# Performance work log

Measured on AMD Instinct MI355X. Metric: run time of the kernel, lower is better.

Reference implementation:

```python
import jax, jax.numpy as jnp
import numpy as np

ALPHA = 2.0
K_HOPS = 3
N_NODES, N_EDGES, IN_DIM = 8192, 131072, 128


def _mlp(coeffs, W0, W1, W2, W3):
    # MLP(n_layers=n_hidden_layers+2=4, relu between, no bias, bn/dropout off in eval)
    h = jax.nn.relu(coeffs @ W0)
    h = jax.nn.relu(h @ W1)
    h = jax.nn.relu(h @ W2)
    return h @ W3  # [N, 1] rotation angles


def _aggregate_k_hop(edge_index, angles):
    # Faithful translation of aggregate_k_hop including its in-place aliasing:
    # enhanced_angles aliases angles, and step_k ACCUMULATES across hops
    # (torch_scatter reduces into the provided out tensor).
    N = angles.shape[0]
    row, col = edge_index[0], edge_index[1]
    f = lambda k: jnp.exp(jnp.asarray(-ALPHA * k, angles.dtype))
    # hop 1: scatter-add over the raw edge list (duplicate edges counted, as in original)
    step = jax.ops.segment_sum(angles[col] * f(1), row, num_segments=N)
    enhanced = angles + step
    # Dense boolean adjacency: composing paths then np.unique(axis=1) is exactly the
    # 'exists a k-step walk' indicator, i.e. boolean adjacency powers.
    adj = jnp.zeros((N, N), jnp.float32).at[row, col].set(1.0)
    P = adj
    for k in range(2, K_HOPS + 1):
        P = ((P @ adj) > 0).astype(jnp.float32)  # unique k-walk pairs
        step = step + f(k) * (P @ enhanced)      # reads angles AFTER previous in-place add
        enhanced = enhanced + step               # step accumulates across hops
    return enhanced


def setup_inputs() -> dict:
    key = jax.random.key(0)
    k0, k1, k2, k3, k4, k5 = jax.random.split(key, 6)
    s = 1.0 / np.sqrt(IN_DIM)
    return {
        "coeffs": jax.random.normal(k0, (N_NODES, IN_DIM), jnp.float32),
        "W0": jax.random.normal(k1, (IN_DIM, IN_DIM), jnp.float32) * s,
        "W1": jax.random.normal(k2, (IN_DIM, IN_DIM), jnp.float32) * s,
        "W2": jax.random.normal(k3, (IN_DIM, IN_DIM), jnp.float32) * s,
        "W3": jax.random.normal(k4, (IN_DIM, 1), jnp.float32) * s,
        "edge_index": jax.random.randint(k5, (2, N_EDGES), 0, N_NODES, dtype=jnp.int32),
    }


def reference(coeffs, W0, W1, W2, W3, edge_index):
    angles = _mlp(coeffs, W0, W1, W2, W3)
    return _aggregate_k_hop(edge_index, angles)  # batch.node_rotation_angles, [N, 1]
```

## Files before the change

kernel.cpp:

```cpp
#include <hip/hip_runtime.h>

constexpr int N    = 8192;
constexpr int NE   = 131072;
constexpr int WPR  = N / 32;
constexpr int MAXD = 64;

#define F1 0.13533528323661270f
#define F2 0.018315638888734179f
#define F3 0.0024787521766663585f

using bf16x8 = __attribute__((ext_vector_type(8))) short;
using f32x4  = __attribute__((ext_vector_type(4))) float;

__device__ __forceinline__ unsigned short f2bf(float f) {
    unsigned int u = __float_as_uint(f);
    u = (u + 0x7FFFu + ((u >> 16) & 1u)) >> 16;
    return (unsigned short)u;
}

__global__ __launch_bounds__(256) void mlp_kernel(
    const float* __restrict__ X,
    const float* __restrict__ W0, const float* __restrict__ W1,
    const float* __restrict__ W2, const float* __restrict__ W3,
    float* __restrict__ angles, float* __restrict__ e1,
    uint4* __restrict__ cntz)
{
    __shared__ unsigned short Xb[32 * 136];
    __shared__ unsigned short Wt[128 * 136];
    __shared__ float part[2][32];

    const int tid  = threadIdx.x;
    const int row0 = blockIdx.x * 32;
    const int w  = tid >> 6, l = tid & 63;
    const int mt = w & 1, nh = w >> 1;
    const int lm = l & 15, lq = l >> 4;

    if (tid < 8) {
        uint4 z; z.x = z.y = z.z = z.w = 0u;
        cntz[blockIdx.x * 8 + tid] = z;
    }

    for (int q = tid; q < 32 * 32; q += 256) {
        float4 v = *(const float4*)&X[row0 * 128 + q * 4];
        ushort4 b;
        b.x = f2bf(v.x); b.y = f2bf(v.y); b.z = f2bf(v.z); b.w = f2bf(v.w);
        *(ushort4*)&Xb[(q >> 5) * 136 + (q & 31) * 4] = b;
    }

    for (int layer = 0; layer < 3; ++layer) {
        const float* __restrict__ W = (layer == 0) ? W0 : (layer == 1) ? W1 : W2;
        for (int it = 0; it < 16; ++it) {
            int flat = it * 256 + tid;
            int n  = flat & 127;
            int k0 = (flat >> 7) << 2;
            ushort4 b;
            b.x = f2bf(W[(k0 + 0) * 128 + n]);
            b.y = f2bf(W[(k0 + 1) * 128 + n]);
            b.z = f2bf(W[(k0 + 2) * 128 + n]);
            b.w = f2bf(W[(k0 + 3) * 128 + n]);
            *(ushort4*)&Wt[n * 136 + k0] = b;
        }
        __syncthreads();

        f32x4 acc[4];
#pragma unroll
        for (int t = 0; t < 4; ++t) acc[t] = (f32x4){0.f, 0.f, 0.f, 0.f};

#pragma unroll
        for (int kc = 0; kc < 4; ++kc) {
            bf16x8 a = *(const bf16x8*)&Xb[(mt * 16 + lm) * 136 + kc * 32 + lq * 8];
#pragma unroll
            for (int t = 0; t < 4; ++t) {
                bf16x8 b = *(const bf16x8*)
                    &Wt[(nh * 64 + t * 16 + lm) * 136 + kc * 32 + lq * 8];
                acc[t] = __builtin_amdgcn_mfma_f32_16x16x32_bf16(a, b, acc[t], 0, 0, 0);
            }
        }

#pragma unroll
        for (int t = 0; t < 4; ++t)
#pragma unroll
            for (int r = 0; r < 4; ++r) acc[t][r] = fmaxf(acc[t][r], 0.0f);

        __syncthreads();

        if (layer < 2) {
#pragma unroll
            for (int t = 0; t < 4; ++t)
#pragma unroll
                for (int r = 0; r < 4; ++r)
                    Xb[(mt * 16 + lq * 4 + r) * 136 + nh * 64 + t * 16 + lm] =
                        f2bf(acc[t][r]);
        } else {
            float p[4] = {0.f, 0.f, 0.f, 0.f};
#pragma unroll
            for (int t = 0; t < 4; ++t) {
                float w3v = W3[nh * 64 + t * 16 + lm];
#pragma unroll
                for (int r = 0; r < 4; ++r) p[r] += acc[t][r] * w3v;
            }
#pragma unroll
            for (int r = 0; r < 4; ++r) {
                p[r] += __shfl_xor(p[r], 1, 64);
                p[r] += __shfl_xor(p[r], 2, 64);
                p[r] += __shfl_xor(p[r], 4, 64);
                p[r] += __shfl_xor(p[r], 8, 64);
            }
            if (lm == 0)
#pragma unroll
                for (int r = 0; r < 4; ++r)
                    part[nh][mt * 16 + lq * 4 + r] = p[r];
            __syncthreads();
            if (tid < 32) {
                float v = part[0][tid] + part[1][tid];
                angles[row0 + tid] = v;
                e1[row0 + tid] = v;
            }
        }
    }
}

__global__ void edges_kernel(const int* __restrict__ ei,
                             const float* __restrict__ angles,
                             float* __restrict__ e1,
                             int* __restrict__ cnt_g,
                             int* __restrict__ nbr_g)
{
    int e = blockIdx.x * blockDim.x + threadIdx.x;
    if (e < NE) {
        int r = ei[e];
        int c = ei[NE + e];
        int p = atomicAdd(&cnt_g[r], 1);
        if (p < MAXD) nbr_g[r * MAXD + p] = c;
        atomicAdd(&e1[r], F1 * angles[c]);
    }
}

__global__ __launch_bounds__(256) void p2_kernel(
    const int* __restrict__ cnt_g, const int* __restrict__ nbr_g,
    unsigned int* __restrict__ P2,
    const float* __restrict__ angles, const float* __restrict__ e1,
    float* __restrict__ e2, float* __restrict__ es)
{
    __shared__ __align__(16) unsigned int bm[4][WPR];
    __shared__ int nbr[4][MAXD];
    __shared__ int nc[4][MAXD];

    const int wv  = threadIdx.x >> 6;
    const int l   = threadIdx.x & 63;
    const int i   = blockIdx.x * 4 + wv;
    const int qq  = l >> 4;
    const int sub = l & 15;

#pragma unroll
    for (int s = 0; s < 4; ++s) bm[wv][s * 64 + l] = 0u;

    const int n = min(cnt_g[i], MAXD);
    if (l < n) {
        int m = nbr_g[i * MAXD + l];
        nbr[wv][l] = m;
        nc[wv][l]  = min(cnt_g[m], MAXD);
    }
    __syncthreads();

    for (int q0 = 0; q0 < n; q0 += 4) {
        int q = q0 + qq;
        int m = 0, c2 = 0;
        if (q < n) { m = nbr[wv][q]; c2 = nc[wv][q]; }
        for (int s = sub; s < c2; s += 16) {
            int id = nbr_g[m * MAXD + s];
            atomicOr(&bm[wv][id >> 5], 1u << (id & 31));
        }
    }
    __syncthreads();

    unsigned int wrd[4];
#pragma unroll
    for (int s = 0; s < 4; ++s) wrd[s] = bm[wv][s * 64 + l];
    uint4 w4; w4.x = wrd[0]; w4.y = wrd[1]; w4.z = wrd[2]; w4.w = wrd[3];
    *(uint4*)&P2[(size_t)i * WPR + 4 * l] = w4;

    float local = 0.0f;
#pragma unroll
    for (int s = 0; s < 4; ++s) {
        unsigned int ww = wrd[s];
        const int base = (s * 64 + l) * 32;
        while (ww) {
            int b = __ffs(ww) - 1;
            ww &= ww - 1;
            local += e1[base + b];
        }
    }
#pragma unroll
    for (int m = 1; m < 64; m <<= 1) local += __shfl_xor(local, m, 64);
    if (l == 0) {
        float e1i = e1[i];
        float s1i = e1i - angles[i];
        float s2v = s1i + F2 * local;
        e2[i] = e1i + s2v;
        es[i] = e1i + 2.0f * s2v;
    }
}

__global__ __launch_bounds__(512) void p3_kernel(
    const unsigned int* __restrict__ P2,
    const int* __restrict__ cnt_g, const int* __restrict__ nbr_g,
    const float* __restrict__ e2, const float* __restrict__ es,
    float* __restrict__ out)
{
    __shared__ float e2s[N];
    __shared__ int nbr[8][MAXD];

    const int tid = threadIdx.x;
    const int wv  = tid >> 6;
    const int l   = tid & 63;
    const int i   = blockIdx.x * 8 + wv;

    for (int q = tid; q < N / 4; q += 512)
        *(float4*)&e2s[q * 4] = *(const float4*)&e2[q * 4];

    const int n = min(cnt_g[i], MAXD);
    if (l < n) nbr[wv][l] = nbr_g[i * MAXD + l];
    __syncthreads();

    unsigned int w[4] = {0u, 0u, 0u, 0u};
    for (int q = 0; q < n; ++q) {
        const uint4* rowp = (const uint4*)(P2 + (size_t)nbr[wv][q] * WPR);
        uint4 r = rowp[l];
        w[0] |= r.x; w[1] |= r.y; w[2] |= r.z; w[3] |= r.w;
    }

    float local = 0.0f;
#pragma unroll
    for (int c = 0; c < 32; ++c) {
        unsigned int wd  = __shfl(w[c >> 3], ((c & 7) << 3) | (l >> 3), 64);
        unsigned int nib = wd >> ((l & 7) * 4);
        float4 v = *(const float4*)&e2s[c * 256 + l * 4];
        local += (nib & 1u) ? v.x : 0.0f;
        local += (nib & 2u) ? v.y : 0.0f;
        local += (nib & 4u) ? v.z : 0.0f;
        local += (nib & 8u) ? v.w : 0.0f;
    }
#pragma unroll
    for (int m = 1; m < 64; m <<= 1) local += __shfl_xor(local, m, 64);
    if (l == 0)
        out[i] = es[i] + F3 * local;
}

extern "C" void kernel_launch(void* const* d_in, const int* in_sizes, int n_in,
                              void* d_out, int out_size, void* d_ws, size_t ws_size,
                              hipStream_t stream)
{
    const float* coeffs = (const float*)d_in[0];
    const float* W0     = (const float*)d_in[1];
    const float* W1     = (const float*)d_in[2];
    const float* W2     = (const float*)d_in[3];
    const float* W3     = (const float*)d_in[4];
    const int*   ei     = (const int*)  d_in[5];
    float* out = (float*)d_out;

    char* ws = (char*)d_ws;
    float*          angles = (float*)(ws + 0 * 32768);
    float*          e2     = (float*)(ws + 1 * 32768);
    float*          es     = (float*)(ws + 2 * 32768);
    int*            nbr_g  = (int*)  (ws + (1u  << 20));
    float*          e1     = (float*)(ws + (4u  << 20));
    int*            cnt_g  = (int*)  (ws + (4u  << 20) + 32768);
    unsigned int*   P2     = (unsigned int*)(ws + (5u  << 20));

    mlp_kernel<<<N / 32, 256, 0, stream>>>(coeffs, W0, W1, W2, W3, angles, e1,
                                           (uint4*)cnt_g);

    edges_kernel<<<NE / 256, 256, 0, stream>>>(ei, angles, e1, cnt_g, nbr_g);
    p2_kernel<<<N / 4, 256, 0, stream>>>(cnt_g, nbr_g, P2, angles, e1, e2, es);
    p3_kernel<<<N / 8, 512, 0, stream>>>(P2, cnt_g, nbr_g, e2, es, out);
}
```

Before: 116.9 us.

## Widen MLP blocks to 512 threads, preload all weights, pair edges per thread

The MLP kernel now runs 512 threads per block, converts all three weight matrices into shared memory once up front, and splits the N dimension across four wave groups. This removes the per-layer weight-load barrier stalls. The cost is about 104 KB of LDS per block, which may limit occupancy. Separately, the edge kernel now handles two edges per thread with int2 loads, halving the grid. The unchanged `tid < 8` zeroing still covers cnt_g correctly.

```diff
diff --git a/kernel.cpp b/kernel.cpp
--- a/kernel.cpp
+++ b/kernel.cpp
@@ -18,7 +18,7 @@
     return (unsigned short)u;
 }
 
-__global__ __launch_bounds__(256) void mlp_kernel(
+__global__ __launch_bounds__(512) void mlp_kernel(
     const float* __restrict__ X,
     const float* __restrict__ W0, const float* __restrict__ W1,
     const float* __restrict__ W2, const float* __restrict__ W3,
@@ -26,8 +26,8 @@
     uint4* __restrict__ cntz)
 {
     __shared__ unsigned short Xb[32 * 136];
-    __shared__ unsigned short Wt[128 * 136];
-    __shared__ float part[2][32];
+    __shared__ unsigned short Wt[3][128 * 136];
+    __shared__ float part[4][32];
 
     const int tid  = threadIdx.x;
     const int row0 = blockIdx.x * 32;
@@ -40,45 +40,46 @@
         cntz[blockIdx.x * 8 + tid] = z;
     }
 
-    for (int q = tid; q < 32 * 32; q += 256) {
+    for (int q = tid; q < 1024; q += 512) {
         float4 v = *(const float4*)&X[row0 * 128 + q * 4];
         ushort4 b;
         b.x = f2bf(v.x); b.y = f2bf(v.y); b.z = f2bf(v.z); b.w = f2bf(v.w);
         *(ushort4*)&Xb[(q >> 5) * 136 + (q & 31) * 4] = b;
     }
 
+    for (int q = tid; q < 3 * 4096; q += 512) {
+        int layer = q >> 12;
+        int flat  = q & 4095;
+        int n  = flat & 127;
+        int k0 = (flat >> 7) << 2;
+        const float* __restrict__ W = (layer == 0) ? W0 : (layer == 1) ? W1 : W2;
+        ushort4 b;
+        b.x = f2bf(W[(k0 + 0) * 128 + n]);
+        b.y = f2bf(W[(k0 + 1) * 128 + n]);
+        b.z = f2bf(W[(k0 + 2) * 128 + n]);
+        b.w = f2bf(W[(k0 + 3) * 128 + n]);
+        *(ushort4*)&Wt[layer][n * 136 + k0] = b;
+    }
+    __syncthreads();
+
     for (int layer = 0; layer < 3; ++layer) {
-        const float* __restrict__ W = (layer == 0) ? W0 : (layer == 1) ? W1 : W2;
-        for (int it = 0; it < 16; ++it) {
-            int flat = it * 256 + tid;
-            int n  = flat & 127;
-            int k0 = (flat >> 7) << 2;
-            ushort4 b;
-            b.x = f2bf(W[(k0 + 0) * 128 + n]);
-            b.y = f2bf(W[(k0 + 1) * 128 + n]);
-            b.z = f2bf(W[(k0 + 2) * 128 + n]);
-            b.w = f2bf(W[(k0 + 3) * 128 + n]);
-            *(ushort4*)&Wt[n * 136 + k0] = b;
-        }
-        __syncthreads();
-
-        f32x4 acc[4];
-#pragma unroll
-        for (int t = 0; t < 4; ++t) acc[t] = (f32x4){0.f, 0.f, 0.f, 0.f};
+        f32x4 acc[2];
+#pragma unroll
+        for (int t = 0; t < 2; ++t) acc[t] = (f32x4){0.f, 0.f, 0.f, 0.f};
 
 #pragma unroll
         for (int kc = 0; kc < 4; ++kc) {
             bf16x8 a = *(const bf16x8*)&Xb[(mt * 16 + lm) * 136 + kc * 32 + lq * 8];
 #pragma unroll
-            for (int t = 0; t < 4; ++t) {
+            for (int t = 0; t < 2; ++t) {
                 bf16x8 b = *(const bf16x8*)
-                    &Wt[(nh * 64 + t * 16 + lm) * 136 + kc * 32 + lq * 8];
+                    &Wt[layer][(nh * 32 + t * 16 + lm) * 136 + kc * 32 + lq * 8];
                 acc[t] = __builtin_amdgcn_mfma_f32_16x16x32_bf16(a, b, acc[t], 0, 0, 0);
             }
         }
 
 #pragma unroll
-        for (int t = 0; t < 4; ++t)
+        for (int t = 0; t < 2; ++t)
 #pragma unroll
             for (int r = 0; r < 4; ++r) acc[t][r] = fmaxf(acc[t][r], 0.0f);
 
@@ -86,16 +87,17 @@
 
         if (layer < 2) {
 #pragma unroll
-            for (int t = 0; t < 4; ++t)
+            for (int t = 0; t < 2; ++t)
 #pragma unroll
                 for (int r = 0; r < 4; ++r)
-                    Xb[(mt * 16 + lq * 4 + r) * 136 + nh * 64 + t * 16 + lm] =
+                    Xb[(mt * 16 + lq * 4 + r) * 136 + nh * 32 + t * 16 + lm] =
                         f2bf(acc[t][r]);
+            __syncthreads();
         } else {
             float p[4] = {0.f, 0.f, 0.f, 0.f};
 #pragma unroll
-            for (int t = 0; t < 4; ++t) {
-                float w3v = W3[nh * 64 + t * 16 + lm];
+            for (int t = 0; t < 2; ++t) {
+                float w3v = W3[nh * 32 + t * 16 + lm];
 #pragma unroll
                 for (int r = 0; r < 4; ++r) p[r] += acc[t][r] * w3v;
             }
@@ -112,7 +114,7 @@
                     part[nh][mt * 16 + lq * 4 + r] = p[r];
             __syncthreads();
             if (tid < 32) {
-                float v = part[0][tid] + part[1][tid];
+                float v = part[0][tid] + part[1][tid] + part[2][tid] + part[3][tid];
                 angles[row0 + tid] = v;
                 e1[row0 + tid] = v;
             }
@@ -126,14 +128,17 @@
                              int* __restrict__ cnt_g,
                              int* __restrict__ nbr_g)
 {
-    int e = blockIdx.x * blockDim.x + threadIdx.x;
-    if (e < NE) {
-        int r = ei[e];
-        int c = ei[NE + e];
-        int p = atomicAdd(&cnt_g[r], 1);
-        if (p < MAXD) nbr_g[r * MAXD + p] = c;
-        atomicAdd(&e1[r], F1 * angles[c]);
-    }
+    int t = blockIdx.x * blockDim.x + threadIdx.x;
+    int2 rr = *(const int2*)&ei[2 * t];
+    int2 cc = *(const int2*)&ei[NE + 2 * t];
+
+    int p0 = atomicAdd(&cnt_g[rr.x], 1);
+    if (p0 < MAXD) nbr_g[rr.x * MAXD + p0] = cc.x;
+    atomicAdd(&e1[rr.x], F1 * angles[cc.x]);
+
+    int p1 = atomicAdd(&cnt_g[rr.y], 1);
+    if (p1 < MAXD) nbr_g[rr.y * MAXD + p1] = cc.y;
+    atomicAdd(&e1[rr.y], F1 * angles[cc.y]);
 }
 
 __global__ __launch_bounds__(256) void p2_kernel(
@@ -268,10 +273,10 @@
     int*            cnt_g  = (int*)  (ws + (4u  << 20) + 32768);
     unsigned int*   P2     = (unsigned int*)(ws + (5u  << 20));
 
-    mlp_kernel<<<N / 32, 256, 0, stream>>>(coeffs, W0, W1, W2, W3, angles, e1,
+    mlp_kernel<<<N / 32, 512, 0, stream>>>(coeffs, W0, W1, W2, W3, angles, e1,
                                            (uint4*)cnt_g);
 
-    edges_kernel<<<NE / 256, 256, 0, stream>>>(ei, angles, e1, cnt_g, nbr_g);
+    edges_kernel<<<NE / 512, 256, 0, stream>>>(ei, angles, e1, cnt_g, nbr_g);
     p2_kernel<<<N / 4, 256, 0, stream>>>(cnt_g, nbr_g, P2, angles, e1, e2, es);
     p3_kernel<<<N / 8, 512, 0, stream>>>(P2, cnt_g, nbr_g, e2, es, out);
 }
```

Result: slower. 119.8 us (+2.5%).

## Fuse edge, P2 and P3 kernels into one persistent kernel with grid barriers

Applied to the files above, without the earlier changes.

Replaces the three graph kernels with a single 256-block, 1024-thread kernel that uses atomic spin grid barriers between the edge-scatter, two-hop bitmap and three-hop reduction phases. Shared memory is unioned across phases, and neighbor lists in the final phase are broadcast by shuffle instead of staged in LDS. The aim is to remove two kernel launch gaps and their tail effects. The cost is relying on all 256 blocks being co-resident, which a normal launch does not guarantee, and lower occupancy from the fixed grid size.

```diff
diff --git a/kernel.cpp b/kernel.cpp
--- a/kernel.cpp
+++ b/kernel.cpp
@@ -16,6 +16,17 @@
     unsigned int u = __float_as_uint(f);
     u = (u + 0x7FFFu + ((u >> 16) & 1u)) >> 16;
     return (unsigned short)u;
+}
+
+__device__ __forceinline__ void grid_barrier(int* bar, int target) {
+    __syncthreads();
+    if (threadIdx.x == 0) {
+        __threadfence();
+        atomicAdd(bar, 1);
+        while (atomicAdd(bar, 0) < target) __builtin_amdgcn_s_sleep(2);
+        __threadfence();
+    }
+    __syncthreads();
 }
 
 __global__ __launch_bounds__(256) void mlp_kernel(
@@ -23,7 +34,7 @@
     const float* __restrict__ W0, const float* __restrict__ W1,
     const float* __restrict__ W2, const float* __restrict__ W3,
     float* __restrict__ angles, float* __restrict__ e1,
-    uint4* __restrict__ cntz)
+    uint4* __restrict__ cntz, int* __restrict__ bar)
 {
     __shared__ unsigned short Xb[32 * 136];
     __shared__ unsigned short Wt[128 * 136];
@@ -39,6 +50,7 @@
         uint4 z; z.x = z.y = z.z = z.w = 0u;
         cntz[blockIdx.x * 8 + tid] = z;
     }
+    if (blockIdx.x == 0 && tid == 0) bar[0] = 0;
 
     for (int q = tid; q < 32 * 32; q += 256) {
         float4 v = *(const float4*)&X[row0 * 128 + q * 4];
@@ -120,131 +132,124 @@
     }
 }
 
-__global__ void edges_kernel(const int* __restrict__ ei,
-                             const float* __restrict__ angles,
-                             float* __restrict__ e1,
-                             int* __restrict__ cnt_g,
-                             int* __restrict__ nbr_g)
+__global__ __launch_bounds__(1024) void fused_graph(
+    const int* __restrict__ ei,
+    const float* __restrict__ angles,
+    float* __restrict__ e1,
+    int* __restrict__ cnt_g, int* __restrict__ nbr_g,
+    unsigned int* __restrict__ P2,
+    float* __restrict__ e2, float* __restrict__ es,
+    float* __restrict__ out, int* __restrict__ bar)
 {
-    int e = blockIdx.x * blockDim.x + threadIdx.x;
-    if (e < NE) {
+    __shared__ __align__(16) union {
+        struct {
+            unsigned int bm[16][WPR];
+            int nbr[16][MAXD];
+            int nc[16][MAXD];
+        } b;
+        float e2s[N];
+    } sm;
+
+    const int tid = threadIdx.x;
+    const int wv  = tid >> 6;
+    const int l   = tid & 63;
+    const int blk = blockIdx.x;
+
+    if (tid < 512) {
+        int e = blk * 512 + tid;
         int r = ei[e];
         int c = ei[NE + e];
         int p = atomicAdd(&cnt_g[r], 1);
         if (p < MAXD) nbr_g[r * MAXD + p] = c;
         atomicAdd(&e1[r], F1 * angles[c]);
     }
-}
-
-__global__ __launch_bounds__(256) void p2_kernel(
-    const int* __restrict__ cnt_g, const int* __restrict__ nbr_g,
-    unsigned int* __restrict__ P2,
-    const float* __restrict__ angles, const float* __restrict__ e1,
-    float* __restrict__ e2, float* __restrict__ es)
-{
-    __shared__ __align__(16) unsigned int bm[4][WPR];
-    __shared__ int nbr[4][MAXD];
-    __shared__ int nc[4][MAXD];
-
-    const int wv  = threadIdx.x >> 6;
-    const int l   = threadIdx.x & 63;
-    const int i   = blockIdx.x * 4 + wv;
-    const int qq  = l >> 4;
-    const int sub = l & 15;
-
-#pragma unroll
-    for (int s = 0; s < 4; ++s) bm[wv][s * 64 + l] = 0u;
-
-    const int n = min(cnt_g[i], MAXD);
-    if (l < n) {
-        int m = nbr_g[i * MAXD + l];
-        nbr[wv][l] = m;
-        nc[wv][l]  = min(cnt_g[m], MAXD);
-    }
+    grid_barrier(bar, 256);
+
+    const int qq = l >> 4, sub = l & 15;
+    for (int rr = 0; rr < 2; ++rr) {
+        const int i = blk * 32 + rr * 16 + wv;
+#pragma unroll
+        for (int s = 0; s < 4; ++s) sm.b.bm[wv][s * 64 + l] = 0u;
+        const int n = min(cnt_g[i], MAXD);
+        if (l < n) {
+            int m = nbr_g[i * MAXD + l];
+            sm.b.nbr[wv][l] = m;
+            sm.b.nc[wv][l]  = min(cnt_g[m], MAXD);
+        }
+        __syncthreads();
+        for (int q0 = 0; q0 < n; q0 += 4) {
+            int q = q0 + qq;
+            int m = 0, c2 = 0;
+            if (q < n) { m = sm.b.nbr[wv][q]; c2 = sm.b.nc[wv][q]; }
+            for (int s = sub; s < c2; s += 16) {
+                int id = nbr_g[m * MAXD + s];
+                atomicOr(&sm.b.bm[wv][id >> 5], 1u << (id & 31));
+            }
+        }
+        __syncthreads();
+
+        unsigned int wrd[4];
+#pragma unroll
+        for (int s = 0; s < 4; ++s) wrd[s] = sm.b.bm[wv][s * 64 + l];
+        uint4 w4; w4.x = wrd[0]; w4.y = wrd[1]; w4.z = wrd[2]; w4.w = wrd[3];
+        *(uint4*)&P2[(size_t)i * WPR + 4 * l] = w4;
+
+        float local = 0.0f;
+#pragma unroll
+        for (int s = 0; s < 4; ++s) {
+            unsigned int ww = wrd[s];
+            const int base = (s * 64 + l) * 32;
+            while (ww) {
+                int b = __ffs(ww) - 1;
+                ww &= ww - 1;
+                local += e1[base + b];
+            }
+        }
+#pragma unroll
+        for (int m = 1; m < 64; m <<= 1) local += __shfl_xor(local, m, 64);
+        if (l == 0) {
+            float e1i = e1[i];
+            float s1i = e1i - angles[i];
+            float s2v = s1i + F2 * local;
+            e2[i] = e1i + s2v;
+            es[i] = e1i + 2.0f * s2v;
+        }
+        __syncthreads();
+    }
+    grid_barrier(bar, 512);
+
+    for (int q = tid; q < N / 4; q += 1024)
+        *(float4*)&sm.e2s[q * 4] = *(const float4*)&e2[q * 4];
     __syncthreads();
 
-    for (int q0 = 0; q0 < n; q0 += 4) {
-        int q = q0 + qq;
-        int m = 0, c2 = 0;
-        if (q < n) { m = nbr[wv][q]; c2 = nc[wv][q]; }
-        for (int s = sub; s < c2; s += 16) {
-            int id = nbr_g[m * MAXD + s];
-            atomicOr(&bm[wv][id >> 5], 1u << (id & 31));
-        }
-    }
-    __syncthreads();
-
-    unsigned int wrd[4];
-#pragma unroll
-    for (int s = 0; s < 4; ++s) wrd[s] = bm[wv][s * 64 + l];
-    uint4 w4; w4.x = wrd[0]; w4.y = wrd[1]; w4.z = wrd[2]; w4.w = wrd[3];
-    *(uint4*)&P2[(size_t)i * WPR + 4 * l] = w4;
-
-    float local = 0.0f;
-#pragma unroll
-    for (int s = 0; s < 4; ++s) {
-        unsigned int ww = wrd[s];
-        const int base = (s * 64 + l) * 32;
-        while (ww) {
-            int b = __ffs(ww) - 1;
-            ww &= ww - 1;
-            local += e1[base + b];
-        }
-    }
-#pragma unroll
-    for (int m = 1; m < 64; m <<= 1) local += __shfl_xor(local, m, 64);
-    if (l == 0) {
-        float e1i = e1[i];
-        float s1i = e1i - angles[i];
-        float s2v = s1i + F2 * local;
-        e2[i] = e1i + s2v;
-        es[i] = e1i + 2.0f * s2v;
-    }
-}
-
-__global__ __launch_bounds__(512) void p3_kernel(
-    const unsigned int* __restrict__ P2,
-    const int* __restrict__ cnt_g, const int* __restrict__ nbr_g,
-    const float* __restrict__ e2, const float* __restrict__ es,
-    float* __restrict__ out)
-{
-    __shared__ float e2s[N];
-    __shared__ int nbr[8][MAXD];
-
-    const int tid = threadIdx.x;
-    const int wv  = tid >> 6;
-    const int l   = tid & 63;
-    const int i   = blockIdx.x * 8 + wv;
-
-    for (int q = tid; q < N / 4; q += 512)
-        *(float4*)&e2s[q * 4] = *(const float4*)&e2[q * 4];
-
-    const int n = min(cnt_g[i], MAXD);
-    if (l < n) nbr[wv][l] = nbr_g[i * MAXD + l];
-    __syncthreads();
-
-    unsigned int w[4] = {0u, 0u, 0u, 0u};
-    for (int q = 0; q < n; ++q) {
-        const uint4* rowp = (const uint4*)(P2 + (size_t)nbr[wv][q] * WPR);
-        uint4 r = rowp[l];
-        w[0] |= r.x; w[1] |= r.y; w[2] |= r.z; w[3] |= r.w;
-    }
-
-    float local = 0.0f;
-#pragma unroll
-    for (int c = 0; c < 32; ++c) {
-        unsigned int wd  = __shfl(w[c >> 3], ((c & 7) << 3) | (l >> 3), 64);
-        unsigned int nib = wd >> ((l & 7) * 4);
-        float4 v = *(const float4*)&e2s[c * 256 + l * 4];
-        local += (nib & 1u) ? v.x : 0.0f;
-        local += (nib & 2u) ? v.y : 0.0f;
-        local += (nib & 4u) ? v.z : 0.0f;
-        local += (nib & 8u) ? v.w : 0.0f;
-    }
-#pragma unroll
-    for (int m = 1; m < 64; m <<= 1) local += __shfl_xor(local, m, 64);
-    if (l == 0)
-        out[i] = es[i] + F3 * local;
+    for (int rr = 0; rr < 2; ++rr) {
+        const int i = blk * 32 + rr * 16 + wv;
+        const int n = min(cnt_g[i], MAXD);
+        int myn = (l < n) ? nbr_g[i * MAXD + l] : 0;
+
+        unsigned int w[4] = {0u, 0u, 0u, 0u};
+        for (int q = 0; q < n; ++q) {
+            int m = __shfl(myn, q, 64);
+            uint4 r = *(const uint4*)(P2 + (size_t)m * WPR + 4 * l);
+            w[0] |= r.x; w[1] |= r.y; w[2] |= r.z; w[3] |= r.w;
+        }
+
+        float local = 0.0f;
+#pragma unroll
+        for (int c = 0; c < 32; ++c) {
+            unsigned int wd  = __shfl(w[c >> 3], ((c & 7) << 3) | (l >> 3), 64);
+            unsigned int nib = wd >> ((l & 7) * 4);
+            float4 v = *(const float4*)&sm.e2s[c * 256 + l * 4];
+            local += (nib & 1u) ? v.x : 0.0f;
+            local += (nib & 2u) ? v.y : 0.0f;
+            local += (nib & 4u) ? v.z : 0.0f;
+            local += (nib & 8u) ? v.w : 0.0f;
+        }
+#pragma unroll
+        for (int m = 1; m < 64; m <<= 1) local += __shfl_xor(local, m, 64);
+        if (l == 0)
+            out[i] = es[i] + F3 * local;
+    }
 }
 
 extern "C" void kernel_launch(void* const* d_in, const int* in_sizes, int n_in,
@@ -263,15 +268,15 @@
     float*          angles = (float*)(ws + 0 * 32768);
     float*          e2     = (float*)(ws + 1 * 32768);
     float*          es     = (float*)(ws + 2 * 32768);
+    int*            bar    = (int*)  (ws + 3 * 32768);
     int*            nbr_g  = (int*)  (ws + (1u  << 20));
     float*          e1     = (float*)(ws + (4u  << 20));
     int*            cnt_g  = (int*)  (ws + (4u  << 20) + 32768);
     unsigned int*   P2     = (unsigned int*)(ws + (5u  << 20));
 
     mlp_kernel<<<N / 32, 256, 0, stream>>>(coeffs, W0, W1, W2, W3, angles, e1,
-                                           (uint4*)cnt_g);
-
-    edges_kernel<<<NE / 256, 256, 0, stream>>>(ei, angles, e1, cnt_g, nbr_g);
-    p2_kernel<<<N / 4, 256, 0, stream>>>(cnt_g, nbr_g, P2, angles, e1, e2, es);
-    p3_kernel<<<N / 8, 512, 0, stream>>>(P2, cnt_g, nbr_g, e2, es, out);
-}
+                                           (uint4*)cnt_g, bar);
+
+    fused_graph<<<256, 1024, 0, stream>>>(ei, angles, e1, cnt_g, nbr_g, P2,
+                                          e2, es, out, bar);
+}
```

Measured after the change: 178.0 us. +52.2%, slower.
